# Kernel optimization log

Measured on AMD Instinct MI355X. Metric: run time of the kernel, lower is better.

Reference implementation:

```python
import jax, jax.numpy as jnp
import numpy as np
from jax import lax

HIDDEN = 128

def setup_inputs() -> dict:
    key = jax.random.key(0)
    ks = jax.random.split(key, 8)
    B, S, V, D = 256, 512, 50000, 300
    x = jax.random.randint(ks[0], (B, S), 0, V, dtype=jnp.int64)
    emb = jax.random.normal(ks[1], (V, D), dtype=jnp.float32)
    s_ih = 1.0 / np.sqrt(HIDDEN)
    W_ih = jax.random.normal(ks[2], (HIDDEN, D), dtype=jnp.float32) * s_ih
    W_hh = jax.random.normal(ks[3], (HIDDEN, HIDDEN), dtype=jnp.float32) * s_ih
    b_ih = jax.random.normal(ks[4], (HIDDEN,), dtype=jnp.float32) * s_ih
    b_hh = jax.random.normal(ks[5], (HIDDEN,), dtype=jnp.float32) * s_ih
    fc_w = jax.random.normal(ks[6], (1, 2 * HIDDEN), dtype=jnp.float32) * (1.0 / np.sqrt(2 * HIDDEN))
    fc_b = jax.random.normal(ks[7], (1,), dtype=jnp.float32) * 0.01
    return {"x": x, "emb": emb, "W_ih": W_ih, "W_hh": W_hh,
            "b_ih": b_ih, "b_hh": b_hh, "fc_w": fc_w, "fc_b": fc_b}

def reference(x, emb, W_ih, W_hh, b_ih, b_hh, fc_w, fc_b):
    # Embedding lookup: [B,S] -> [B,S,D]
    xe = emb[x]
    # Precompute input projection for all timesteps: [B,S,H]
    xp = jnp.einsum('bsd,hd->bsh', xe, W_ih) + b_ih
    B = xp.shape[0]
    h0 = jnp.zeros((B, HIDDEN), dtype=xp.dtype)

    def step(h, xt):  # xt: [B,H]
        h = jnp.tanh(xt + h @ W_hh.T + b_hh)
        return h, h

    _, outs = lax.scan(step, h0, xp.transpose(1, 0, 2))  # outs: [S,B,H]
    outs = outs.transpose(1, 0, 2)  # [B,S,H]
    pooled = jnp.concatenate([outs.max(axis=1), outs.mean(axis=1)], axis=-1)  # [B,2H]
    return pooled @ fc_w.T + fc_b  # [B,1]
```

## Files before the change

kernel.cpp:

```cpp
#include <hip/hip_runtime.h>

#define HID    128
#define SEQ    512
#define BATCH  256
#define DIM    300
#define VOCAB  50000

typedef short bf16x8 __attribute__((ext_vector_type(8)));
typedef float f32x4  __attribute__((ext_vector_type(4)));

#define KP     320
#define LST    328
#define TROWS  32
#define NTILES ((VOCAB + TROWS - 1) / TROWS)

__device__ __forceinline__ unsigned bf16_rtne(float v)
{
    unsigned u = __float_as_uint(v);
    return (u + 0x7FFFu + ((u >> 16) & 1u)) >> 16;
}

__global__ __launch_bounds__(512)
void proj_persist(const float* __restrict__ emb,
                  const float* __restrict__ Wih,
                  const float* __restrict__ bih,
                  const float* __restrict__ bhh,
                  float* __restrict__ P)
{
    __shared__ unsigned short Bt[128 * LST];
    __shared__ unsigned short At[2 * TROWS * LST];

    const int t   = threadIdx.x;
    const int bid = blockIdx.x;

    for (int c = t; c < 128 * 40; c += 512) {
        const int row = c / 40;
        const int ch  = c - row * 40;
        const float* src = Wih + (size_t)row * DIM;
        const int k0 = ch * 8;
        unsigned p0, p1, p2, p3;
        if (k0 + 8 <= DIM) {
            const float4 a = *(const float4*)(src + k0);
            const float4 b = *(const float4*)(src + k0 + 4);
            p0 = bf16_rtne(a.x) | (bf16_rtne(a.y) << 16);
            p1 = bf16_rtne(a.z) | (bf16_rtne(a.w) << 16);
            p2 = bf16_rtne(b.x) | (bf16_rtne(b.y) << 16);
            p3 = bf16_rtne(b.z) | (bf16_rtne(b.w) << 16);
        } else {
            unsigned q[8];
            #pragma unroll
            for (int e = 0; e < 8; ++e) {
                const int k = k0 + e;
                q[e] = (k < DIM) ? bf16_rtne(src[k]) : 0u;
            }
            p0 = q[0] | (q[1] << 16);  p1 = q[2] | (q[3] << 16);
            p2 = q[4] | (q[5] << 16);  p3 = q[6] | (q[7] << 16);
        }
        uint4 o = {p0, p1, p2, p3};
        *(uint4*)(&Bt[row * LST + k0]) = o;
    }

#define STAGE_EMB(tl, bf) do {                                                \
        const int v0_ = (tl) * TROWS;                                         \
        for (int c = t; c < TROWS * 40; c += 512) {                           \
            const int row = c / 40;                                           \
            const int ch  = c - row * 40;                                     \
            int grow = v0_ + row; if (grow > VOCAB - 1) grow = VOCAB - 1;     \
            const float* src = emb + (size_t)grow * DIM;                      \
            const int k0 = ch * 8;                                            \
            unsigned p0, p1, p2, p3;                                          \
            if (k0 + 8 <= DIM) {                                              \
                const float4 a = *(const float4*)(src + k0);                  \
                const float4 b = *(const float4*)(src + k0 + 4);              \
                p0 = bf16_rtne(a.x) | (bf16_rtne(a.y) << 16);                 \
                p1 = bf16_rtne(a.z) | (bf16_rtne(a.w) << 16);                 \
                p2 = bf16_rtne(b.x) | (bf16_rtne(b.y) << 16);                 \
                p3 = bf16_rtne(b.z) | (bf16_rtne(b.w) << 16);                 \
            } else {                                                          \
                unsigned q[8];                                                \
                _Pragma("unroll")                                             \
                for (int e = 0; e < 8; ++e) {                                 \
                    const int k = k0 + e;                                     \
                    q[e] = (k < DIM) ? bf16_rtne(src[k]) : 0u;                \
                }                                                             \
                p0 = q[0] | (q[1] << 16);  p1 = q[2] | (q[3] << 16);          \
                p2 = q[4] | (q[5] << 16);  p3 = q[6] | (q[7] << 16);          \
            }                                                                 \
            uint4 o = {p0, p1, p2, p3};                                       \
            *(uint4*)(&At[(bf) * (TROWS * LST) + row * LST + k0]) = o;        \
        }                                                                     \
    } while (0)

    const int lane = t & 63;
    const int w    = t >> 6;
    const int mt   = w >> 2;
    const int np   = w & 3;
    const int lm   = lane & 15;
    const int kg   = lane >> 4;

    STAGE_EMB(bid, 0);
    __syncthreads();

    int buf = 0;
    for (int tile = bid; tile < NTILES; tile += 256) {
        if (tile + 256 < NTILES) STAGE_EMB(tile + 256, buf ^ 1);

        const unsigned short* arow = &At[buf * (TROWS * LST)
                                         + (mt * 16 + lm) * LST + kg * 8];
        const unsigned short* brow = &Bt[(np * 32 + lm) * LST + kg * 8];

        f32x4 acc0 = {0.f,0.f,0.f,0.f}, acc1 = {0.f,0.f,0.f,0.f};
        #pragma unroll
        for (int k0 = 0; k0 < KP; k0 += 32) {
            const bf16x8 af = *(const bf16x8*)(arow + k0);
            const bf16x8 b0 = *(const bf16x8*)(brow + k0);
            const bf16x8 b1 = *(const bf16x8*)(brow + 16 * LST + k0);
            acc0 = __builtin_amdgcn_mfma_f32_16x16x32_bf16(af, b0, acc0, 0, 0, 0);
            acc1 = __builtin_amdgcn_mfma_f32_16x16x32_bf16(af, b1, acc1, 0, 0, 0);
        }

        const int rbase = tile * TROWS + mt * 16 + kg * 4;
        #pragma unroll
        for (int nt2 = 0; nt2 < 2; ++nt2) {
            const int h = (np * 2 + nt2) * 16 + lm;
            const float bb = bih[h] + bhh[h];
            const f32x4 a = nt2 ? acc1 : acc0;
            #pragma unroll
            for (int r = 0; r < 4; ++r) {
                const int row = rbase + r;
                if (row < VOCAB) P[(size_t)row * HID + h] = a[r] + bb;
            }
        }

        __syncthreads();
        buf ^= 1;
    }
#undef STAGE_EMB
}

__device__ __forceinline__ float quad_sum(float v)
{
    int x1 = __builtin_amdgcn_update_dpp(0, __float_as_int(v), 0xB1, 0xF, 0xF, true);
    v += __int_as_float(x1);
    int x2 = __builtin_amdgcn_update_dpp(0, __float_as_int(v), 0x4E, 0xF, 0xF, true);
    v += __int_as_float(x2);
    return v;
}

__global__ __launch_bounds__(512)
void rnn_kernel(const int* __restrict__ x,
                const float* __restrict__ Whh,
                const float* __restrict__ P,
                const float* __restrict__ fcw,
                const float* __restrict__ fcb,
                float* __restrict__ out)
{
    __shared__ float h0b[HID];
    __shared__ float h1b[HID];
    __shared__ int   toff[SEQ];
    __shared__ float xb[2 * 64 * HID];
    __shared__ float red[HID];

    const int t  = threadIdx.x;
    const int b  = blockIdx.x;
    const int i  = t >> 2;
    const int kq = t & 3;

    toff[t] = x[b * SEQ + t] * HID;
    if (t < HID) h0b[t] = 0.f;

    float4 w[8];
    #pragma unroll
    for (int j = 0; j < 8; ++j) {
        const int pj = (j + 2 * kq) & 7;
        w[j] = *(const float4*)(Whh + (size_t)i * HID + kq * 32 + pj * 4);
    }
    __syncthreads();

#define STAGE(cn) do {                                                        \
        const int w_ = t >> 6, l_ = t & 63;                                   \
        const int base_ = ((cn) & 1) * (64 * HID);                            \
        _Pragma("unroll")                                                     \
        for (int q_ = 0; q_ < 4; ++q_) {                                      \
            const int row_ = w_ * 8 + q_ * 2 + (l_ >> 5);                     \
            const int col_ = (l_ & 31) * 4;                                   \
            const int off_ = toff[(cn) * 64 + row_] + col_;                   \
            const float4 v_ = *(const float4*)(P + off_);                     \
            *(float4*)(&xb[base_ + row_ * HID + col_]) = v_;                  \
        }                                                                     \
    } while (0)

    STAGE(0);
    __syncthreads();

    float hmax = -3.0e38f, hsum = 0.f;

#define STEP(HRD, HWR, XPTR, SOFF) do {                                       \
        const float xt = (XPTR)[(SOFF) * HID];                                \
        float ac0=0.f,ac1=0.f,ac2=0.f,ac3=0.f,ac4=0.f,ac5=0.f,ac6=0.f,ac7=0.f;\
        _Pragma("unroll")                                                     \
        for (int j = 0; j < 8; ++j) {                                         \
            const int pj = (j + 2 * kq) & 7;                                  \
            const float4 h4 = *(const float4*)((HRD) + kq * 32 + pj * 4);     \
            float* ap = (j==0)?&ac0:(j==1)?&ac1:(j==2)?&ac2:(j==3)?&ac3       \
                       :(j==4)?&ac4:(j==5)?&ac5:(j==6)?&ac6:&ac7;             \
            *ap = fmaf(w[j].x, h4.x, *ap);                                    \
            *ap = fmaf(w[j].y, h4.y, *ap);                                    \
            *ap = fmaf(w[j].z, h4.z, *ap);                                    \
            *ap = fmaf(w[j].w, h4.w, *ap);                                    \
        }                                                                     \
        float acc = ((ac0+ac1)+(ac2+ac3)) + ((ac4+ac5)+(ac6+ac7));            \
        acc = quad_sum(acc);                                                  \
        const float z = xt + acc;                                             \
        const float e = __builtin_amdgcn_exp2f(z * 2.8853900817779268f);      \
        const float hnew = fmaf(-2.f, __builtin_amdgcn_rcpf(e + 1.f), 1.f);   \
        hmax = fmaxf(hmax, hnew);                                             \
        hsum += hnew;                                                         \
        (HWR)[i] = hnew;                                                      \
        __syncthreads();                                                      \
    } while (0)

    for (int c = 0; c < 8; ++c) {
        if (c < 7) STAGE(c + 1);
        const float* xp = &xb[(c & 1) * (64 * HID) + i];
        #pragma unroll 4
        for (int u = 0; u < 32; ++u) {
            STEP(h0b, h1b, xp, u * 2);
            STEP(h1b, h0b, xp, u * 2 + 1);
        }
    }
#undef STEP
#undef STAGE

    if (kq == 0)
        red[i] = fcw[i] * hmax + fcw[HID + i] * (hsum * (1.f / 512.f));
    __syncthreads();
    if (t < 64) {
        float v = red[t] + red[t + 64];
        #pragma unroll
        for (int m = 32; m >= 1; m >>= 1) v += __shfl_xor(v, m);
        if (t == 0) out[b] = v + fcb[0];
    }
}

extern "C" void kernel_launch(void* const* d_in, const int* in_sizes, int n_in,
                              void* d_out, int out_size, void* d_ws, size_t ws_size,
                              hipStream_t stream)
{
    const int*   x   = (const int*)  d_in[0];
    const float* emb = (const float*)d_in[1];
    const float* Wih = (const float*)d_in[2];
    const float* Whh = (const float*)d_in[3];
    const float* bih = (const float*)d_in[4];
    const float* bhh = (const float*)d_in[5];
    const float* fcw = (const float*)d_in[6];
    const float* fcb = (const float*)d_in[7];

    float* P = (float*)d_ws;

    proj_persist<<<256, 512, 0, stream>>>(emb, Wih, bih, bhh, P);
    rnn_kernel<<<BATCH, 512, 0, stream>>>(x, Whh, P, fcw, fcb, (float*)d_out);
}
```

Before: 197.8 us.

## Process two batch rows per RNN block to halve barriers per step

The RNN kernel now handles two independent sequences per workgroup and interleaves their timesteps, so each __syncthreads covers two recurrent updates instead of one. The grid halves to 128 blocks, and the staging buffers shrink to 32-step chunks per sequence. This targets barrier latency on the serial recurrence. In exchange it uses only half the workgroups on a GPU with 256 CUs and lengthens each step's dependent chain.

```diff
diff --git a/kernel.cpp b/kernel.cpp
--- a/kernel.cpp
+++ b/kernel.cpp
@@ -148,26 +148,28 @@
 }
 
 __global__ __launch_bounds__(512)
-void rnn_kernel(const int* __restrict__ x,
-                const float* __restrict__ Whh,
-                const float* __restrict__ P,
-                const float* __restrict__ fcw,
-                const float* __restrict__ fcb,
-                float* __restrict__ out)
-{
-    __shared__ float h0b[HID];
-    __shared__ float h1b[HID];
-    __shared__ int   toff[SEQ];
-    __shared__ float xb[2 * 64 * HID];
+void rnn2_kernel(const int* __restrict__ x,
+                 const float* __restrict__ Whh,
+                 const float* __restrict__ P,
+                 const float* __restrict__ fcw,
+                 const float* __restrict__ fcb,
+                 float* __restrict__ out)
+{
+    __shared__ float hA0[HID], hA1[HID];
+    __shared__ float hB0[HID], hB1[HID];
+    __shared__ int   toffA[SEQ], toffB[SEQ];
+    __shared__ float xbA[2 * 32 * HID];
+    __shared__ float xbB[2 * 32 * HID];
     __shared__ float red[HID];
 
     const int t  = threadIdx.x;
-    const int b  = blockIdx.x;
+    const int b2 = blockIdx.x * 2;
     const int i  = t >> 2;
     const int kq = t & 3;
 
-    toff[t] = x[b * SEQ + t] * HID;
-    if (t < HID) h0b[t] = 0.f;
+    toffA[t] = x[(size_t)b2 * SEQ + t] * HID;
+    toffB[t] = x[(size_t)(b2 + 1) * SEQ + t] * HID;
+    if (t < HID) { hA0[t] = 0.f; hB0[t] = 0.f; }
 
     float4 w[8];
     #pragma unroll
@@ -177,25 +179,26 @@
     }
     __syncthreads();
 
-#define STAGE(cn) do {                                                        \
-        const int w_ = t >> 6, l_ = t & 63;                                   \
-        const int base_ = ((cn) & 1) * (64 * HID);                            \
+#define STAGE2(TOFF, XB, cn, bf) do {                                         \
         _Pragma("unroll")                                                     \
-        for (int q_ = 0; q_ < 4; ++q_) {                                      \
-            const int row_ = w_ * 8 + q_ * 2 + (l_ >> 5);                     \
-            const int col_ = (l_ & 31) * 4;                                   \
-            const int off_ = toff[(cn) * 64 + row_] + col_;                   \
+        for (int q_ = 0; q_ < 2; ++q_) {                                      \
+            const int idx_ = t + q_ * 512;                                    \
+            const int row_ = idx_ >> 5;                                       \
+            const int c4_  = idx_ & 31;                                       \
+            const int off_ = (TOFF)[(cn) * 32 + row_] + c4_ * 4;              \
             const float4 v_ = *(const float4*)(P + off_);                     \
-            *(float4*)(&xb[base_ + row_ * HID + col_]) = v_;                  \
+            *(float4*)(&(XB)[(bf) * (32 * HID) + row_ * HID + c4_ * 4]) = v_; \
         }                                                                     \
     } while (0)
 
-    STAGE(0);
-    __syncthreads();
-
-    float hmax = -3.0e38f, hsum = 0.f;
-
-#define STEP(HRD, HWR, XPTR, SOFF) do {                                       \
+    STAGE2(toffA, xbA, 0, 0);
+    STAGE2(toffB, xbB, 0, 0);
+    __syncthreads();
+
+    float hmaxA = -3.0e38f, hsumA = 0.f;
+    float hmaxB = -3.0e38f, hsumB = 0.f;
+
+#define STEP2(HRD, HWR, XPTR, SOFF, HMAX, HSUM) do {                          \
         const float xt = (XPTR)[(SOFF) * HID];                                \
         float ac0=0.f,ac1=0.f,ac2=0.f,ac3=0.f,ac4=0.f,ac5=0.f,ac6=0.f,ac7=0.f;\
         _Pragma("unroll")                                                     \
@@ -214,32 +217,49 @@
         const float z = xt + acc;                                             \
         const float e = __builtin_amdgcn_exp2f(z * 2.8853900817779268f);      \
         const float hnew = fmaf(-2.f, __builtin_amdgcn_rcpf(e + 1.f), 1.f);   \
-        hmax = fmaxf(hmax, hnew);                                             \
-        hsum += hnew;                                                         \
+        HMAX = fmaxf(HMAX, hnew);                                             \
+        HSUM += hnew;                                                         \
         (HWR)[i] = hnew;                                                      \
-        __syncthreads();                                                      \
     } while (0)
 
-    for (int c = 0; c < 8; ++c) {
-        if (c < 7) STAGE(c + 1);
-        const float* xp = &xb[(c & 1) * (64 * HID) + i];
-        #pragma unroll 4
-        for (int u = 0; u < 32; ++u) {
-            STEP(h0b, h1b, xp, u * 2);
-            STEP(h1b, h0b, xp, u * 2 + 1);
-        }
-    }
-#undef STEP
-#undef STAGE
+    for (int c = 0; c < 16; ++c) {
+        if (c < 15) {
+            STAGE2(toffA, xbA, c + 1, (c + 1) & 1);
+            STAGE2(toffB, xbB, c + 1, (c + 1) & 1);
+        }
+        const float* xpA = &xbA[(c & 1) * (32 * HID) + i];
+        const float* xpB = &xbB[(c & 1) * (32 * HID) + i];
+        #pragma unroll 2
+        for (int u = 0; u < 16; ++u) {
+            STEP2(hA0, hA1, xpA, u * 2,     hmaxA, hsumA);
+            STEP2(hB0, hB1, xpB, u * 2,     hmaxB, hsumB);
+            __syncthreads();
+            STEP2(hA1, hA0, xpA, u * 2 + 1, hmaxA, hsumA);
+            STEP2(hB1, hB0, xpB, u * 2 + 1, hmaxB, hsumB);
+            __syncthreads();
+        }
+    }
+#undef STEP2
+#undef STAGE2
 
     if (kq == 0)
-        red[i] = fcw[i] * hmax + fcw[HID + i] * (hsum * (1.f / 512.f));
+        red[i] = fcw[i] * hmaxA + fcw[HID + i] * (hsumA * (1.f / 512.f));
     __syncthreads();
     if (t < 64) {
         float v = red[t] + red[t + 64];
         #pragma unroll
         for (int m = 32; m >= 1; m >>= 1) v += __shfl_xor(v, m);
-        if (t == 0) out[b] = v + fcb[0];
+        if (t == 0) out[b2] = v + fcb[0];
+    }
+    __syncthreads();
+    if (kq == 0)
+        red[i] = fcw[i] * hmaxB + fcw[HID + i] * (hsumB * (1.f / 512.f));
+    __syncthreads();
+    if (t < 64) {
+        float v = red[t] + red[t + 64];
+        #pragma unroll
+        for (int m = 32; m >= 1; m >>= 1) v += __shfl_xor(v, m);
+        if (t == 0) out[b2 + 1] = v + fcb[0];
     }
 }
 
@@ -259,5 +279,5 @@
     float* P = (float*)d_ws;
 
     proj_persist<<<256, 512, 0, stream>>>(emb, Wih, bih, bhh, P);
-    rnn_kernel<<<BATCH, 512, 0, stream>>>(x, Whh, P, fcw, fcb, (float*)d_out);
-}
+    rnn2_kernel<<<BATCH / 2, 512, 0, stream>>>(x, Whh, P, fcw, fcb, (float*)d_out);
+}
```

Result: slower. 406.3 us (+105.4%).

## Use fp16 packed dot products for recurrent matvec with two rows per thread group

Applied to the files above, without the earlier changes.

Stores the hidden state in shared memory as fp16 and converts W_hh rows to packed fp16 registers, computing the recurrent matvec with fdot2 instructions. Each 8-thread group now handles two output rows with a 16-element K slice, using an 8-lane DPP reduction. This is meant to cut the FMA count and the LDS read volume on the serial critical path of each timestep. It trades away precision: the weights use round-toward-zero fp16 and the hidden state is fp16, which may add error over 512 steps.

```diff
diff --git a/kernel.cpp b/kernel.cpp
--- a/kernel.cpp
+++ b/kernel.cpp
@@ -8,6 +8,7 @@
 
 typedef short bf16x8 __attribute__((ext_vector_type(8)));
 typedef float f32x4  __attribute__((ext_vector_type(4)));
+typedef __fp16 half2_t __attribute__((ext_vector_type(2)));
 
 #define KP     320
 #define LST    328
@@ -146,6 +147,17 @@
     v += __int_as_float(x2);
     return v;
 }
+__device__ __forceinline__ float oct_sum(float v)
+{
+    v = quad_sum(v);
+    int m = __builtin_amdgcn_update_dpp(0, __float_as_int(v), 0x141, 0xF, 0xF, true);
+    return v + __int_as_float(m);
+}
+
+__device__ __forceinline__ half2_t u2h(unsigned u)
+{
+    union { unsigned u; half2_t h; } c; c.u = u; return c.h;
+}
 
 __global__ __launch_bounds__(512)
 void rnn_kernel(const int* __restrict__ x,
@@ -155,25 +167,35 @@
                 const float* __restrict__ fcb,
                 float* __restrict__ out)
 {
-    __shared__ float h0b[HID];
-    __shared__ float h1b[HID];
+    __shared__ __align__(16) unsigned short h0b[HID];
+    __shared__ __align__(16) unsigned short h1b[HID];
     __shared__ int   toff[SEQ];
     __shared__ float xb[2 * 64 * HID];
     __shared__ float red[HID];
 
     const int t  = threadIdx.x;
     const int b  = blockIdx.x;
-    const int i  = t >> 2;
-    const int kq = t & 3;
+    const int o  = t >> 3;
+    const int ke = t & 7;
+    const int r0 = 2 * o;
+    const int r1 = 2 * o + 1;
 
     toff[t] = x[b * SEQ + t] * HID;
-    if (t < HID) h0b[t] = 0.f;
-
-    float4 w[8];
-    #pragma unroll
-    for (int j = 0; j < 8; ++j) {
-        const int pj = (j + 2 * kq) & 7;
-        w[j] = *(const float4*)(Whh + (size_t)i * HID + kq * 32 + pj * 4);
+    if (t < HID) h0b[t] = 0;
+
+    half2_t wh0[8], wh1[8];
+    {
+        const float* wr0 = Whh + (size_t)r0 * HID + ke * 16;
+        const float* wr1 = Whh + (size_t)r1 * HID + ke * 16;
+        #pragma unroll
+        for (int j = 0; j < 4; ++j) {
+            const float4 a = *(const float4*)(wr0 + j * 4);
+            wh0[2*j]   = __builtin_amdgcn_cvt_pkrtz(a.x, a.y);
+            wh0[2*j+1] = __builtin_amdgcn_cvt_pkrtz(a.z, a.w);
+            const float4 c = *(const float4*)(wr1 + j * 4);
+            wh1[2*j]   = __builtin_amdgcn_cvt_pkrtz(c.x, c.y);
+            wh1[2*j+1] = __builtin_amdgcn_cvt_pkrtz(c.z, c.w);
+        }
     }
     __syncthreads();
 
@@ -193,36 +215,53 @@
     STAGE(0);
     __syncthreads();
 
-    float hmax = -3.0e38f, hsum = 0.f;
+    float hmax0 = -3.0e38f, hsum0 = 0.f;
+    float hmax1 = -3.0e38f, hsum1 = 0.f;
 
 #define STEP(HRD, HWR, XPTR, SOFF) do {                                       \
-        const float xt = (XPTR)[(SOFF) * HID];                                \
-        float ac0=0.f,ac1=0.f,ac2=0.f,ac3=0.f,ac4=0.f,ac5=0.f,ac6=0.f,ac7=0.f;\
-        _Pragma("unroll")                                                     \
-        for (int j = 0; j < 8; ++j) {                                         \
-            const int pj = (j + 2 * kq) & 7;                                  \
-            const float4 h4 = *(const float4*)((HRD) + kq * 32 + pj * 4);     \
-            float* ap = (j==0)?&ac0:(j==1)?&ac1:(j==2)?&ac2:(j==3)?&ac3       \
-                       :(j==4)?&ac4:(j==5)?&ac5:(j==6)?&ac6:&ac7;             \
-            *ap = fmaf(w[j].x, h4.x, *ap);                                    \
-            *ap = fmaf(w[j].y, h4.y, *ap);                                    \
-            *ap = fmaf(w[j].z, h4.z, *ap);                                    \
-            *ap = fmaf(w[j].w, h4.w, *ap);                                    \
+        const float xt0 = (XPTR)[(SOFF) * HID];                               \
+        const float xt1 = (XPTR)[(SOFF) * HID + 1];                           \
+        const uint4 qa = *(const uint4*)((HRD) + ke * 16);                    \
+        const uint4 qb = *(const uint4*)((HRD) + ke * 16 + 8);                \
+        float a00 = 0.f, a01 = 0.f, a10 = 0.f, a11 = 0.f;                     \
+        a00 = __builtin_amdgcn_fdot2(wh0[0], u2h(qa.x), a00, false);          \
+        a10 = __builtin_amdgcn_fdot2(wh1[0], u2h(qa.x), a10, false);          \
+        a00 = __builtin_amdgcn_fdot2(wh0[1], u2h(qa.y), a00, false);          \
+        a10 = __builtin_amdgcn_fdot2(wh1[1], u2h(qa.y), a10, false);          \
+        a00 = __builtin_amdgcn_fdot2(wh0[2], u2h(qa.z), a00, false);          \
+        a10 = __builtin_amdgcn_fdot2(wh1[2], u2h(qa.z), a10, false);          \
+        a00 = __builtin_amdgcn_fdot2(wh0[3], u2h(qa.w), a00, false);          \
+        a10 = __builtin_amdgcn_fdot2(wh1[3], u2h(qa.w), a10, false);          \
+        a01 = __builtin_amdgcn_fdot2(wh0[4], u2h(qb.x), a01, false);          \
+        a11 = __builtin_amdgcn_fdot2(wh1[4], u2h(qb.x), a11, false);          \
+        a01 = __builtin_amdgcn_fdot2(wh0[5], u2h(qb.y), a01, false);          \
+        a11 = __builtin_amdgcn_fdot2(wh1[5], u2h(qb.y), a11, false);          \
+        a01 = __builtin_amdgcn_fdot2(wh0[6], u2h(qb.z), a01, false);          \
+        a11 = __builtin_amdgcn_fdot2(wh1[6], u2h(qb.z), a11, false);          \
+        a01 = __builtin_amdgcn_fdot2(wh0[7], u2h(qb.w), a01, false);          \
+        a11 = __builtin_amdgcn_fdot2(wh1[7], u2h(qb.w), a11, false);          \
+        const float s0 = oct_sum(a00 + a01);                                  \
+        const float s1 = oct_sum(a10 + a11);                                  \
+        const float z0 = xt0 + s0;                                            \
+        const float z1 = xt1 + s1;                                            \
+        const float e0 = __builtin_amdgcn_exp2f(z0 * 2.8853900817779268f);    \
+        const float h0n = fmaf(-2.f, __builtin_amdgcn_rcpf(e0 + 1.f), 1.f);   \
+        const float e1 = __builtin_amdgcn_exp2f(z1 * 2.8853900817779268f);    \
+        const float h1n = fmaf(-2.f, __builtin_amdgcn_rcpf(e1 + 1.f), 1.f);   \
+        hmax0 = fmaxf(hmax0, h0n); hsum0 += h0n;                              \
+        hmax1 = fmaxf(hmax1, h1n); hsum1 += h1n;                              \
+        if ((ke & 3) == 0) {                                                  \
+            const int hi_ = ke >> 2;                                          \
+            union { __fp16 f; unsigned short u; } cv_;                        \
+            cv_.f = (__fp16)(hi_ ? h1n : h0n);                                \
+            (HWR)[hi_ ? r1 : r0] = cv_.u;                                     \
         }                                                                     \
-        float acc = ((ac0+ac1)+(ac2+ac3)) + ((ac4+ac5)+(ac6+ac7));            \
-        acc = quad_sum(acc);                                                  \
-        const float z = xt + acc;                                             \
-        const float e = __builtin_amdgcn_exp2f(z * 2.8853900817779268f);      \
-        const float hnew = fmaf(-2.f, __builtin_amdgcn_rcpf(e + 1.f), 1.f);   \
-        hmax = fmaxf(hmax, hnew);                                             \
-        hsum += hnew;                                                         \
-        (HWR)[i] = hnew;                                                      \
         __syncthreads();                                                      \
     } while (0)
 
     for (int c = 0; c < 8; ++c) {
         if (c < 7) STAGE(c + 1);
-        const float* xp = &xb[(c & 1) * (64 * HID) + i];
+        const float* xp = &xb[(c & 1) * (64 * HID) + r0];
         #pragma unroll 4
         for (int u = 0; u < 32; ++u) {
             STEP(h0b, h1b, xp, u * 2);
@@ -232,8 +271,13 @@
 #undef STEP
 #undef STAGE
 
-    if (kq == 0)
-        red[i] = fcw[i] * hmax + fcw[HID + i] * (hsum * (1.f / 512.f));
+    if ((ke & 3) == 0) {
+        const int hi = ke >> 2;
+        const int r  = hi ? r1 : r0;
+        const float hm = hi ? hmax1 : hmax0;
+        const float hs = hi ? hsum1 : hsum0;
+        red[r] = fcw[r] * hm + fcw[HID + r] * (hs * (1.f / 512.f));
+    }
     __syncthreads();
     if (t < 64) {
         float v = red[t] + red[t + 64];
```

Result: no change. 200.8 us (+1.5%).

## Batch 16 sequences per block and compute recurrence with bf16 MFMA

Applied to the files above, without the earlier changes.

Replaces the per-batch fp32 FMA recurrence kernel with a kernel where each block processes 16 sequences and computes W_hh·h using bf16 16x16x32 MFMA instructions, with W_hh held in registers and h stored as swizzled bf16 in LDS. Input projections are gathered directly from global memory with a three-step register prefetch instead of LDS staging. This aims to shorten the per-step serial dependency chain, at the cost of using only 16 blocks and reduced precision for the hidden state and weights.

```diff
diff --git a/kernel.cpp b/kernel.cpp
--- a/kernel.cpp
+++ b/kernel.cpp
@@ -18,6 +18,18 @@
 {
     unsigned u = __float_as_uint(v);
     return (u + 0x7FFFu + ((u >> 16) & 1u)) >> 16;
+}
+
+__device__ __forceinline__ bf16x8 pack_bf8(const float* src)
+{
+    union { uint4 u; bf16x8 v; } c;
+    const float4 a = *(const float4*)(src);
+    const float4 b = *(const float4*)(src + 4);
+    c.u.x = bf16_rtne(a.x) | (bf16_rtne(a.y) << 16);
+    c.u.y = bf16_rtne(a.z) | (bf16_rtne(a.w) << 16);
+    c.u.z = bf16_rtne(b.x) | (bf16_rtne(b.y) << 16);
+    c.u.w = bf16_rtne(b.z) | (bf16_rtne(b.w) << 16);
+    return c.v;
 }
 
 __global__ __launch_bounds__(512)
@@ -138,108 +150,141 @@
 #undef STAGE_EMB
 }
 
-__device__ __forceinline__ float quad_sum(float v)
-{
-    int x1 = __builtin_amdgcn_update_dpp(0, __float_as_int(v), 0xB1, 0xF, 0xF, true);
-    v += __int_as_float(x1);
-    int x2 = __builtin_amdgcn_update_dpp(0, __float_as_int(v), 0x4E, 0xF, 0xF, true);
-    v += __int_as_float(x2);
-    return v;
-}
-
-__global__ __launch_bounds__(512)
-void rnn_kernel(const int* __restrict__ x,
-                const float* __restrict__ Whh,
-                const float* __restrict__ P,
-                const float* __restrict__ fcw,
-                const float* __restrict__ fcb,
-                float* __restrict__ out)
-{
-    __shared__ float h0b[HID];
-    __shared__ float h1b[HID];
-    __shared__ int   toff[SEQ];
-    __shared__ float xb[2 * 64 * HID];
-    __shared__ float red[HID];
+__device__ __forceinline__ float tanh_fast(float z)
+{
+    const float e = __builtin_amdgcn_exp2f(z * 2.8853900817779268f);
+    return fmaf(-2.f, __builtin_amdgcn_rcpf(e + 1.f), 1.f);
+}
+
+__global__ __launch_bounds__(256)
+void rnn_mfma(const int* __restrict__ x,
+              const float* __restrict__ Whh,
+              const float* __restrict__ P,
+              const float* __restrict__ fcw,
+              const float* __restrict__ fcb,
+              float* __restrict__ out)
+{
+    __shared__ unsigned short Hb[2][16 * 128];
+    __shared__ int   toff2[SEQ * 16];
+    __shared__ float red[256];
 
     const int t  = threadIdx.x;
-    const int b  = blockIdx.x;
-    const int i  = t >> 2;
-    const int kq = t & 3;
-
-    toff[t] = x[b * SEQ + t] * HID;
-    if (t < HID) h0b[t] = 0.f;
-
-    float4 w[8];
-    #pragma unroll
-    for (int j = 0; j < 8; ++j) {
-        const int pj = (j + 2 * kq) & 7;
-        w[j] = *(const float4*)(Whh + (size_t)i * HID + kq * 32 + pj * 4);
-    }
+    const int b0 = blockIdx.x * 16;
+    const int w  = t >> 6;
+    const int m  = t & 15;
+    const int g  = (t >> 4) & 3;
+
+    for (int c = t; c < SEQ * 16; c += 256)
+        toff2[c] = x[(size_t)(b0 + (c & 15)) * SEQ + (c >> 4)] * HID;
+    ((uint4*)Hb[0])[t] = uint4{0, 0, 0, 0};
+
+    const int nA = 32 * w + m;
+    const int nB = nA + 16;
+    const bf16x8 wa00 = pack_bf8(Whh + (size_t)nA * HID +  0 + g * 8);
+    const bf16x8 wa01 = pack_bf8(Whh + (size_t)nA * HID + 32 + g * 8);
+    const bf16x8 wa02 = pack_bf8(Whh + (size_t)nA * HID + 64 + g * 8);
+    const bf16x8 wa03 = pack_bf8(Whh + (size_t)nA * HID + 96 + g * 8);
+    const bf16x8 wa10 = pack_bf8(Whh + (size_t)nB * HID +  0 + g * 8);
+    const bf16x8 wa11 = pack_bf8(Whh + (size_t)nB * HID + 32 + g * 8);
+    const bf16x8 wa12 = pack_bf8(Whh + (size_t)nB * HID + 64 + g * 8);
+    const bf16x8 wa13 = pack_bf8(Whh + (size_t)nB * HID + 96 + g * 8);
     __syncthreads();
 
-#define STAGE(cn) do {                                                        \
-        const int w_ = t >> 6, l_ = t & 63;                                   \
-        const int base_ = ((cn) & 1) * (64 * HID);                            \
-        _Pragma("unroll")                                                     \
-        for (int q_ = 0; q_ < 4; ++q_) {                                      \
-            const int row_ = w_ * 8 + q_ * 2 + (l_ >> 5);                     \
-            const int col_ = (l_ & 31) * 4;                                   \
-            const int off_ = toff[(cn) * 64 + row_] + col_;                   \
-            const float4 v_ = *(const float4*)(P + off_);                     \
-            *(float4*)(&xb[base_ + row_ * HID + col_]) = v_;                  \
-        }                                                                     \
-    } while (0)
-
-    STAGE(0);
-    __syncthreads();
-
-    float hmax = -3.0e38f, hsum = 0.f;
-
-#define STEP(HRD, HWR, XPTR, SOFF) do {                                       \
-        const float xt = (XPTR)[(SOFF) * HID];                                \
-        float ac0=0.f,ac1=0.f,ac2=0.f,ac3=0.f,ac4=0.f,ac5=0.f,ac6=0.f,ac7=0.f;\
-        _Pragma("unroll")                                                     \
-        for (int j = 0; j < 8; ++j) {                                         \
-            const int pj = (j + 2 * kq) & 7;                                  \
-            const float4 h4 = *(const float4*)((HRD) + kq * 32 + pj * 4);     \
-            float* ap = (j==0)?&ac0:(j==1)?&ac1:(j==2)?&ac2:(j==3)?&ac3       \
-                       :(j==4)?&ac4:(j==5)?&ac5:(j==6)?&ac6:&ac7;             \
-            *ap = fmaf(w[j].x, h4.x, *ap);                                    \
-            *ap = fmaf(w[j].y, h4.y, *ap);                                    \
-            *ap = fmaf(w[j].z, h4.z, *ap);                                    \
-            *ap = fmaf(w[j].w, h4.w, *ap);                                    \
-        }                                                                     \
-        float acc = ((ac0+ac1)+(ac2+ac3)) + ((ac4+ac5)+(ac6+ac7));            \
-        acc = quad_sum(acc);                                                  \
-        const float z = xt + acc;                                             \
-        const float e = __builtin_amdgcn_exp2f(z * 2.8853900817779268f);      \
-        const float hnew = fmaf(-2.f, __builtin_amdgcn_rcpf(e + 1.f), 1.f);   \
-        hmax = fmaxf(hmax, hnew);                                             \
-        hsum += hnew;                                                         \
-        (HWR)[i] = hnew;                                                      \
+    const int swz  = (m & 7) << 4;
+    const int rb   = m * 256;
+    const int rdo0 = rb + ((  0 + g * 16) ^ swz);
+    const int rdo1 = rb + (( 64 + g * 16) ^ swz);
+    const int rdo2 = rb + ((128 + g * 16) ^ swz);
+    const int rdo3 = rb + ((192 + g * 16) ^ swz);
+    const int n00  = 32 * w + g * 4;
+    const int n01  = n00 + 16;
+    const int wro0 = rb + ((n00 * 2) ^ swz);
+    const int wro1 = rb + ((n01 * 2) ^ swz);
+
+    float hmax00 = -3.0e38f, hmax01 = -3.0e38f, hmax02 = -3.0e38f, hmax03 = -3.0e38f;
+    float hmax10 = -3.0e38f, hmax11 = -3.0e38f, hmax12 = -3.0e38f, hmax13 = -3.0e38f;
+    float hsum00 = 0.f, hsum01 = 0.f, hsum02 = 0.f, hsum03 = 0.f;
+    float hsum10 = 0.f, hsum11 = 0.f, hsum12 = 0.f, hsum13 = 0.f;
+
+    float4 xA0, xA1, xB0, xB1, xC0, xC1, xD0, xD1;
+    { const int to = toff2[0 * 16 + m]; xA0 = *(const float4*)(P + to + n00); xA1 = *(const float4*)(P + to + n01); }
+    { const int to = toff2[1 * 16 + m]; xB0 = *(const float4*)(P + to + n00); xB1 = *(const float4*)(P + to + n01); }
+    { const int to = toff2[2 * 16 + m]; xC0 = *(const float4*)(P + to + n00); xC1 = *(const float4*)(P + to + n01); }
+
+#define RSTEP(RD, XM0, XM1, XO0, XO1, SLD) do {                               \
+        { const int to_ = toff2[(SLD) * 16 + m];                              \
+          XO0 = *(const float4*)(P + to_ + n00);                              \
+          XO1 = *(const float4*)(P + to_ + n01); }                            \
+        const char* hrd_ = (const char*)Hb[RD];                               \
+        char*       hwr_ = (char*)Hb[(RD) ^ 1];                               \
+        const bf16x8 q0_ = *(const bf16x8*)(hrd_ + rdo0);                     \
+        const bf16x8 q1_ = *(const bf16x8*)(hrd_ + rdo1);                     \
+        const bf16x8 q2_ = *(const bf16x8*)(hrd_ + rdo2);                     \
+        const bf16x8 q3_ = *(const bf16x8*)(hrd_ + rdo3);                     \
+        f32x4 a0_ = {0.f, 0.f, 0.f, 0.f};                                     \
+        f32x4 a1_ = {0.f, 0.f, 0.f, 0.f};                                     \
+        a0_ = __builtin_amdgcn_mfma_f32_16x16x32_bf16(wa00, q0_, a0_, 0,0,0); \
+        a1_ = __builtin_amdgcn_mfma_f32_16x16x32_bf16(wa10, q0_, a1_, 0,0,0); \
+        a0_ = __builtin_amdgcn_mfma_f32_16x16x32_bf16(wa01, q1_, a0_, 0,0,0); \
+        a1_ = __builtin_amdgcn_mfma_f32_16x16x32_bf16(wa11, q1_, a1_, 0,0,0); \
+        a0_ = __builtin_amdgcn_mfma_f32_16x16x32_bf16(wa02, q2_, a0_, 0,0,0); \
+        a1_ = __builtin_amdgcn_mfma_f32_16x16x32_bf16(wa12, q2_, a1_, 0,0,0); \
+        a0_ = __builtin_amdgcn_mfma_f32_16x16x32_bf16(wa03, q3_, a0_, 0,0,0); \
+        a1_ = __builtin_amdgcn_mfma_f32_16x16x32_bf16(wa13, q3_, a1_, 0,0,0); \
+        const float h00_ = tanh_fast(a0_[0] + (XM0).x);                       \
+        const float h01_ = tanh_fast(a0_[1] + (XM0).y);                       \
+        const float h02_ = tanh_fast(a0_[2] + (XM0).z);                       \
+        const float h03_ = tanh_fast(a0_[3] + (XM0).w);                       \
+        const float h10_ = tanh_fast(a1_[0] + (XM1).x);                       \
+        const float h11_ = tanh_fast(a1_[1] + (XM1).y);                       \
+        const float h12_ = tanh_fast(a1_[2] + (XM1).z);                       \
+        const float h13_ = tanh_fast(a1_[3] + (XM1).w);                       \
+        hmax00 = fmaxf(hmax00, h00_); hsum00 += h00_;                         \
+        hmax01 = fmaxf(hmax01, h01_); hsum01 += h01_;                         \
+        hmax02 = fmaxf(hmax02, h02_); hsum02 += h02_;                         \
+        hmax03 = fmaxf(hmax03, h03_); hsum03 += h03_;                         \
+        hmax10 = fmaxf(hmax10, h10_); hsum10 += h10_;                         \
+        hmax11 = fmaxf(hmax11, h11_); hsum11 += h11_;                         \
+        hmax12 = fmaxf(hmax12, h12_); hsum12 += h12_;                         \
+        hmax13 = fmaxf(hmax13, h13_); hsum13 += h13_;                         \
+        uint2 wv0_, wv1_;                                                     \
+        wv0_.x = bf16_rtne(h00_) | (bf16_rtne(h01_) << 16);                   \
+        wv0_.y = bf16_rtne(h02_) | (bf16_rtne(h03_) << 16);                   \
+        wv1_.x = bf16_rtne(h10_) | (bf16_rtne(h11_) << 16);                   \
+        wv1_.y = bf16_rtne(h12_) | (bf16_rtne(h13_) << 16);                   \
+        *(uint2*)(hwr_ + wro0) = wv0_;                                        \
+        *(uint2*)(hwr_ + wro1) = wv1_;                                        \
         __syncthreads();                                                      \
     } while (0)
 
-    for (int c = 0; c < 8; ++c) {
-        if (c < 7) STAGE(c + 1);
-        const float* xp = &xb[(c & 1) * (64 * HID) + i];
-        #pragma unroll 4
-        for (int u = 0; u < 32; ++u) {
-            STEP(h0b, h1b, xp, u * 2);
-            STEP(h1b, h0b, xp, u * 2 + 1);
-        }
+    for (int s = 0; s < SEQ; s += 4) {
+        const int p3 = (s + 3 < SEQ) ? s + 3 : SEQ - 1;
+        const int p4 = (s + 4 < SEQ) ? s + 4 : SEQ - 1;
+        const int p5 = (s + 5 < SEQ) ? s + 5 : SEQ - 1;
+        const int p6 = (s + 6 < SEQ) ? s + 6 : SEQ - 1;
+        RSTEP(0, xA0, xA1, xD0, xD1, p3);
+        RSTEP(1, xB0, xB1, xA0, xA1, p4);
+        RSTEP(0, xC0, xC1, xB0, xB1, p5);
+        RSTEP(1, xD0, xD1, xC0, xC1, p6);
     }
-#undef STEP
-#undef STAGE
-
-    if (kq == 0)
-        red[i] = fcw[i] * hmax + fcw[HID + i] * (hsum * (1.f / 512.f));
+#undef RSTEP
+
+    float part = 0.f;
+    part += fcw[n00 + 0] * hmax00 + fcw[HID + n00 + 0] * (hsum00 * (1.f / 512.f));
+    part += fcw[n00 + 1] * hmax01 + fcw[HID + n00 + 1] * (hsum01 * (1.f / 512.f));
+    part += fcw[n00 + 2] * hmax02 + fcw[HID + n00 + 2] * (hsum02 * (1.f / 512.f));
+    part += fcw[n00 + 3] * hmax03 + fcw[HID + n00 + 3] * (hsum03 * (1.f / 512.f));
+    part += fcw[n01 + 0] * hmax10 + fcw[HID + n01 + 0] * (hsum10 * (1.f / 512.f));
+    part += fcw[n01 + 1] * hmax11 + fcw[HID + n01 + 1] * (hsum11 * (1.f / 512.f));
+    part += fcw[n01 + 2] * hmax12 + fcw[HID + n01 + 2] * (hsum12 * (1.f / 512.f));
+    part += fcw[n01 + 3] * hmax13 + fcw[HID + n01 + 3] * (hsum13 * (1.f / 512.f));
+    red[t] = part;
     __syncthreads();
-    if (t < 64) {
-        float v = red[t] + red[t + 64];
+    if (t < 16) {
+        float v = 0.f;
         #pragma unroll
-        for (int m = 32; m >= 1; m >>= 1) v += __shfl_xor(v, m);
-        if (t == 0) out[b] = v + fcb[0];
+        for (int j = 0; j < 16; ++j) v += red[t + 16 * j];
+        out[b0 + t] = v + fcb[0];
     }
 }
 
@@ -259,5 +304,5 @@
     float* P = (float*)d_ws;
 
     proj_persist<<<256, 512, 0, stream>>>(emb, Wih, bih, bhh, P);
-    rnn_kernel<<<BATCH, 512, 0, stream>>>(x, Whh, P, fcw, fcb, (float*)d_out);
-}
+    rnn_mfma<<<16, 256, 0, stream>>>(x, Whh, P, fcw, fcb, (float*)d_out);
+}
```

Result: slower. 249.6 us (+26.2%).
